# Optimization experiments

Measured on AMD Instinct MI355X. Metric: run time of the kernel, lower is better.

Reference implementation:

```python
import jax, jax.numpy as jnp
import numpy as np

N = 50000
E = 800000
IO = 128
HID = 256
KQ = 256
EPS = 1e-5


def setup_inputs() -> dict:
    key = jax.random.key(0)
    ks = jax.random.split(key, 16)
    def w(k, shape, fan_in):
        return jax.random.normal(k, shape, dtype=jnp.float32) / np.sqrt(fan_in)
    x0 = jax.random.normal(ks[0], (N, IO), dtype=jnp.float32)
    edges = jax.random.randint(ks[1], (2, E), 0, N, dtype=jnp.int64)
    return {
        "x0": x0,
        "edges": edges,
        "Wq1": w(ks[2], (IO, KQ), IO), "Wk1": w(ks[3], (IO, KQ), IO),
        "Wv1": w(ks[4], (IO, HID), IO), "Wr1": w(ks[5], (IO, HID), IO),
        "b1": jnp.zeros((HID,), jnp.float32),
        "g1": jnp.ones((HID,), jnp.float32), "be1": jnp.zeros((HID,), jnp.float32),
        "Wq2": w(ks[6], (HID, KQ), HID), "Wk2": w(ks[7], (HID, KQ), HID),
        "Wv2": w(ks[8], (HID, IO), HID), "Wr2": w(ks[9], (HID, IO), HID),
        "b2": jnp.zeros((IO,), jnp.float32),
        "g2": jnp.ones((IO,), jnp.float32), "be2": jnp.zeros((IO,), jnp.float32),
    }


def _transformer_conv(x, src, dst, Wq, Wk, Wv, Wr, b, n):
    # single-head graph transformer conv (PyG TransformerConv style)
    q = x @ Wq                      # [n, kq]
    k = x @ Wk                      # [n, kq]
    v = x @ Wv                      # [n, out]
    scale = 1.0 / np.sqrt(Wq.shape[1])
    logits = jnp.sum(q[dst] * k[src], axis=-1) * scale   # [E]
    m = jax.lax.stop_gradient(jax.ops.segment_max(logits, dst, num_segments=n))
    m = jnp.where(jnp.isfinite(m), m, 0.0)
    e = jnp.exp(logits - m[dst])                          # [E]
    s = jax.ops.segment_sum(e, dst, num_segments=n)       # [n]
    alpha = e / jnp.maximum(s[dst], 1e-16)                # [E]
    agg = jax.ops.segment_sum(alpha[:, None] * v[src], dst, num_segments=n)
    return agg + x @ Wr + b


def _batch_norm(x, gamma, beta):
    mu = jnp.mean(x, axis=0)
    var = jnp.mean((x - mu) ** 2, axis=0)  # biased var, as torch BN training
    return (x - mu) * jax.lax.rsqrt(var + EPS) * gamma + beta


def reference(x0, edges, Wq1, Wk1, Wv1, Wr1, b1, g1, be1,
              Wq2, Wk2, Wv2, Wr2, b2, g2, be2):
    src, dst = edges[0], edges[1]
    n = x0.shape[0]
    x = _transformer_conv(x0, src, dst, Wq1, Wk1, Wv1, Wr1, b1, n)
    x = jax.nn.relu(_batch_norm(x, g1, be1))
    x = _transformer_conv(x, src, dst, Wq2, Wk2, Wv2, Wr2, b2, n)
    x = _batch_norm(x, g2, be2)
    return jax.nn.relu(x + x0)
```

## Files before the change

### kernel.cpp

```cpp
#include <hip/hip_runtime.h>
#include <stdint.h>

typedef unsigned short ushort_t;

__device__ __forceinline__ float bf2f(unsigned short u) {
  union { unsigned int i; float f; } c; c.i = ((unsigned int)u) << 16; return c.f;
}
__device__ __forceinline__ unsigned short f2bf(float f) {
  union { float f; unsigned int i; } c; c.f = f;
  unsigned int r = c.i + 0x7FFFu + ((c.i >> 16) & 1u);
  return (unsigned short)(r >> 16);
}
__device__ __forceinline__ float relu_nanprop(float v) { return (v < 0.f) ? 0.f : v; }

__device__ __forceinline__ void async_copy16(const void* g, void* l) {
  __builtin_amdgcn_global_load_lds(
      (const __attribute__((address_space(1))) unsigned int*)(uintptr_t)g,
      (__attribute__((address_space(3))) unsigned int*)(uintptr_t)l,
      16, 0, 0);
}

typedef __attribute__((ext_vector_type(8))) short s16x8;
typedef __attribute__((ext_vector_type(4))) float f32x4;

__device__ __forceinline__ int edge_at(const void* edges, int wide, int idx) {
  if (wide) return (int)((const long long*)edges)[idx];
  return ((const int*)edges)[idx];
}

__global__ void setup_kernel(int* __restrict__ zreg2, int N,
                             const int* __restrict__ e32, int n32, int* __restrict__ eflag,
                             const unsigned int* __restrict__ x, int nw, int* __restrict__ fF) {
  int b = blockIdx.x, tid = threadIdx.x;
  if (b < 256) {
    int total = 2 * N + 1024;
    for (int i = b * 256 + tid; i < total; i += 256 * 256) zreg2[i] = 0;
  } else if (b == 256) {
    __shared__ int any;
    if (tid == 0) any = 0;
    __syncthreads();
    for (int i = tid; i < 4096; i += 256) {
      int idx = 2 * i + 1;
      if (idx < n32 && e32[idx] != 0) any = 1;
    }
    __syncthreads();
    if (tid == 0) eflag[0] = (any == 0) ? 1 : 0;
  } else {
    __shared__ int cnt;
    if (tid == 0) cnt = 0;
    __syncthreads();
    int local = 0;
    for (int i = tid; i < 4096 && i < nw; i += 256) {
      unsigned int low = x[i] & 0xFFFFu;
      unsigned int e = (low >> 7) & 0xFFu;
      if (low != 0u && (e < 96u || e > 144u)) local++;
    }
    atomicAdd(&cnt, local);
    __syncthreads();
    if (tid == 0) fF[0] = (cnt > 1024) ? 1 : 0;
  }
}

__global__ void cvt_all_kernel(const void* __restrict__ x0, ushort_t* __restrict__ x0b, int nx,
                               const void* p0, const void* p1, const void* p2,
                               const void* p3, const void* p4, const void* p5,
                               ushort_t* o0, ushort_t* o1, ushort_t* o2,
                               ushort_t* o3, ushort_t* o4, ushort_t* o5,
                               const void* W10, const void* W11, const void* W12, const void* W13,
                               ushort_t* __restrict__ Wq1b, ushort_t* __restrict__ Wk1b,
                               ushort_t* __restrict__ wcatB1, ushort_t* __restrict__ wcatV1,
                               const void* W20, const void* W21, const void* W22, const void* W23,
                               ushort_t* __restrict__ Wq2b, ushort_t* __restrict__ Wk2b,
                               ushort_t* __restrict__ wcatB2, ushort_t* __restrict__ wcatV2,
                               const void* __restrict__ edges, int* __restrict__ deg,
                               int E, int Nn,
                               const int* __restrict__ eflag, const int* __restrict__ fF) {
  int b = blockIdx.x, tid = threadIdx.x;
  int f = fF[0];
  if (b < 4096) {
    for (int i = b * 256 + tid; i < nx; i += 4096 * 256)
      x0b[i] = f ? f2bf(((const float*)x0)[i]) : ((const ushort_t*)x0)[i];
  } else if (b == 4096) {
    const void* ins[6] = {p0, p1, p2, p3, p4, p5};
    ushort_t* outs[6] = {o0, o1, o2, o3, o4, o5};
    const int segs[7] = {0, 256, 512, 768, 896, 1024, 1152};
    for (int i = tid; i < 1152; i += 256) {
      int s = 0;
      while (i >= segs[s + 1]) s++;
      int li = i - segs[s];
      outs[s][li] = f ? f2bf(((const float*)ins[s])[li]) : ((const ushort_t*)ins[s])[li];
    }
  } else if (b < 4609) {
    for (int i = (b - 4097) * 256 + tid; i < 131072; i += 512 * 256) {
      if (i < 32768) {
        Wq1b[i] = f ? f2bf(((const float*)W10)[i]) : ((const ushort_t*)W10)[i];
      } else if (i < 65536) {
        int r = i - 32768;
        Wk1b[r] = f ? f2bf(((const float*)W11)[r]) : ((const ushort_t*)W11)[r];
      } else if (i < 98304) {
        int rem = i - 65536, k = rem >> 8, c = rem & 255;
        ushort_t v = f ? f2bf(((const float*)W13)[rem]) : ((const ushort_t*)W13)[rem];
        wcatB1[(size_t)(128 + c) * 128 + k] = v;
      } else {
        int rem = i - 98304, k = rem >> 8, c = rem & 255;
        ushort_t v = f ? f2bf(((const float*)W12)[rem]) : ((const ushort_t*)W12)[rem];
        wcatV1[(size_t)c * 128 + k] = v;
      }
    }
  } else if (b < 5121) {
    for (int i = (b - 4609) * 256 + tid; i < 196608; i += 512 * 256) {
      if (i < 65536) {
        Wq2b[i] = f ? f2bf(((const float*)W20)[i]) : ((const ushort_t*)W20)[i];
      } else if (i < 131072) {
        int r = i - 65536;
        Wk2b[r] = f ? f2bf(((const float*)W21)[r]) : ((const ushort_t*)W21)[r];
      } else if (i < 163840) {
        int rem = i - 131072, k = rem >> 7, c = rem & 127;
        ushort_t v = f ? f2bf(((const float*)W23)[rem]) : ((const ushort_t*)W23)[rem];
        wcatB2[(size_t)(256 + c) * 256 + k] = v;
      } else {
        int rem = i - 163840, k = rem >> 7, c = rem & 127;
        ushort_t v = f ? f2bf(((const float*)W22)[rem]) : ((const ushort_t*)W22)[rem];
        wcatV2[(size_t)c * 256 + k] = v;
      }
    }
  } else {
    int wide = eflag[0];
    for (int e = (b - 5121) * 256 + tid; e < E; e += 1024 * 256) {
      int d = edge_at(edges, wide, E + e);
      if (d < 0) d = 0; if (d >= Nn) d = Nn - 1;
      atomicAdd(&deg[d], 1);
    }
  }
}

__global__ void chunk_sum_kernel(const int* __restrict__ deg, int* __restrict__ csum, int n) {
  int b = blockIdx.x, t = threadIdx.x, i = b * 256 + t;
  int v = (i < n) ? deg[i] : 0;
  __shared__ int ws[4];
#pragma unroll
  for (int o = 32; o > 0; o >>= 1) v += __shfl_down(v, o);
  if ((t & 63) == 0) ws[t >> 6] = v;
  __syncthreads();
  if (t == 0) csum[b] = ws[0] + ws[1] + ws[2] + ws[3];
}

__global__ void scan_small_kernel(const int* __restrict__ csum, int* __restrict__ cpre,
                                  int nc, int* __restrict__ offs, int N) {
  __shared__ int tmp[256];
  int t = threadIdx.x;
  int v = (t < nc) ? csum[t] : 0;
  tmp[t] = v;
  __syncthreads();
  for (int off = 1; off < 256; off <<= 1) {
    int x = (t >= off) ? tmp[t - off] : 0;
    __syncthreads();
    tmp[t] += x;
    __syncthreads();
  }
  if (t < nc) cpre[t] = tmp[t] - v;
  if (t == 255) offs[N] = tmp[255];
}

__global__ void scan_final_kernel(const int* __restrict__ deg, const int* __restrict__ cpre,
                                  int* __restrict__ offs, int n) {
  int b = blockIdx.x, t = threadIdx.x, i = b * 256 + t;
  __shared__ int tmp[256];
  int v = (i < n) ? deg[i] : 0;
  tmp[t] = v;
  __syncthreads();
  for (int off = 1; off < 256; off <<= 1) {
    int x = (t >= off) ? tmp[t - off] : 0;
    __syncthreads();
    tmp[t] += x;
    __syncthreads();
  }
  if (i < n) offs[i] = cpre[b] + tmp[t] - v;
}

__global__ void scatter_kernel(const void* __restrict__ edges, const int* __restrict__ flag,
                               const int* __restrict__ offs, int* __restrict__ fill,
                               int* __restrict__ srcS, int E, int Nn) {
  int wide = flag[0];
  for (int e = blockIdx.x * blockDim.x + threadIdx.x; e < E; e += gridDim.x * blockDim.x) {
    int s = edge_at(edges, wide, e);
    int d = edge_at(edges, wide, E + e);
    if (d < 0) d = 0; if (d >= Nn) d = Nn - 1;
    if (s < 0) s = 0; if (s >= Nn) s = Nn - 1;
    int p = offs[d] + atomicAdd(&fill[d], 1);
    if (p < 0) p = 0; if (p >= E) p = E - 1;
    srcS[p] = s;
  }
}

__global__ __launch_bounds__(256)
void gemm4_kernel(const ushort_t* __restrict__ A, const ushort_t* __restrict__ BT,
                  ushort_t* __restrict__ o0, ushort_t* __restrict__ o1,
                  ushort_t* __restrict__ o2, ushort_t* __restrict__ o3,
                  const ushort_t* __restrict__ bias3,
                  int M, int K, int NC, int b0, int b1, int b2, int accum) {
  __shared__ __align__(16) ushort_t As[128 * 32];
  __shared__ __align__(16) ushort_t Bs[128 * 32];
  int tid = threadIdx.x;
  int lane = tid & 63, wave = tid >> 6;
  int tm = blockIdx.x * 128, tn = blockIdx.y * 128;
  int wm = (wave >> 1) * 64, wn = (wave & 1) * 64;
  int q = lane >> 4, l = lane & 15;
  f32x4 acc[4][4];
#pragma unroll
  for (int a = 0; a < 4; a++)
#pragma unroll
    for (int b = 0; b < 4; b++) acc[a][b] = (f32x4){0.f, 0.f, 0.f, 0.f};

  int lrow = lane >> 2, c8 = (lane & 3) * 8;
  for (int k0 = 0; k0 < K; k0 += 32) {
#pragma unroll
    for (int t = 0; t < 2; t++) {
      int chunk = t * 4 + wave;
      int row = chunk * 16 + lrow;
      int ra = tm + row; if (ra > M - 1) ra = M - 1;
      async_copy16(&A[(size_t)ra * K + k0 + c8], &As[chunk * 512]);
      async_copy16(&BT[(size_t)(tn + row) * K + k0 + c8], &Bs[chunk * 512]);
    }
    __syncthreads();
    s16x8 af[4], bfr[4];
#pragma unroll
    for (int mf = 0; mf < 4; mf++) af[mf] = *(const s16x8*)&As[(wm + mf * 16 + l) * 32 + q * 8];
#pragma unroll
    for (int nf = 0; nf < 4; nf++) bfr[nf] = *(const s16x8*)&Bs[(wn + nf * 16 + l) * 32 + q * 8];
#pragma unroll
    for (int mf = 0; mf < 4; mf++)
#pragma unroll
      for (int nf = 0; nf < 4; nf++)
        acc[mf][nf] = __builtin_amdgcn_mfma_f32_16x16x32_bf16(af[mf], bfr[nf], acc[mf][nf], 0, 0, 0);
    __syncthreads();
  }
  ushort_t* op; int sbase, w; bool addb = false;
  if (tn < b0)      { op = o0; sbase = 0;  w = b0; }
  else if (tn < b1) { op = o1; sbase = b0; w = b1 - b0; }
  else if (tn < b2) { op = o2; sbase = b1; w = b2 - b1; }
  else              { op = o3; sbase = b2; w = NC - b2; addb = true; }
  int lc0 = tn + wn - sbase + l;
  float bv[4];
#pragma unroll
  for (int nf = 0; nf < 4; nf++) bv[nf] = addb ? bf2f(bias3[lc0 + nf * 16]) : 0.f;
#pragma unroll
  for (int mf = 0; mf < 4; mf++) {
#pragma unroll
    for (int j = 0; j < 4; j++) {
      int r = tm + wm + mf * 16 + q * 4 + j;
      if (r < M) {
#pragma unroll
        for (int nf = 0; nf < 4; nf++) {
          size_t idx = (size_t)r * w + lc0 + nf * 16;
          float prev = accum ? bf2f(op[idx]) : 0.f;
          op[idx] = f2bf(acc[mf][nf][j] + bv[nf] + prev);
        }
      }
    }
  }
}

__global__ __launch_bounds__(256)
void attn_kernel(const ushort_t* __restrict__ qt, const ushort_t* __restrict__ x,
                 const int* __restrict__ offs, const int* __restrict__ srcS,
                 ushort_t* __restrict__ aggb, int D, int Nn) {
  int lane = threadIdx.x & 63, wave = threadIdx.x >> 6;
  int n = blockIdx.x * 4 + wave;
  if (n >= Nn) return;
  int g = lane >> 4, sub = lane & 15;

  int e0 = offs[n], e1 = offs[n + 1];
  float wsum = 0.f;

  if (D == 128) {
    s16x8 qv = __builtin_nontemporal_load((const s16x8*)(qt + (size_t)n * 128 + sub * 8));
    float qf[8];
#pragma unroll
    for (int i = 0; i < 8; i++) qf[i] = bf2f((unsigned short)qv[i]);
    float acc[8];
#pragma unroll
    for (int i = 0; i < 8; i++) acc[i] = 0.f;
    int j = e0;
    s16x8 xc;
    bool have = (j + 4 <= e1);
    if (have) {
      int s = __builtin_nontemporal_load(srcS + j + g);
      if (s < 0 || s >= Nn) s = 0;
      xc = *(const s16x8*)(x + (size_t)s * 128 + sub * 8);
    }
    for (; j + 8 <= e1; j += 4) {
      int s2 = __builtin_nontemporal_load(srcS + j + 4 + g);
      if (s2 < 0 || s2 >= Nn) s2 = 0;
      s16x8 xn = *(const s16x8*)(x + (size_t)s2 * 128 + sub * 8);
      float p = 0.f;
#pragma unroll
      for (int i = 0; i < 8; i++) p += qf[i] * bf2f((unsigned short)xc[i]);
      p += __shfl_xor(p, 1); p += __shfl_xor(p, 2);
      p += __shfl_xor(p, 4); p += __shfl_xor(p, 8);
      float w = __expf(p * 0.0625f);
      wsum += w;
#pragma unroll
      for (int i = 0; i < 8; i++) acc[i] += w * bf2f((unsigned short)xc[i]);
      xc = xn;
    }
    if (have) {
      float p = 0.f;
#pragma unroll
      for (int i = 0; i < 8; i++) p += qf[i] * bf2f((unsigned short)xc[i]);
      p += __shfl_xor(p, 1); p += __shfl_xor(p, 2);
      p += __shfl_xor(p, 4); p += __shfl_xor(p, 8);
      float w = __expf(p * 0.0625f);
      wsum += w;
#pragma unroll
      for (int i = 0; i < 8; i++) acc[i] += w * bf2f((unsigned short)xc[i]);
      j += 4;
    }
    int rem = e1 - j;
    if (rem > 0) {
      bool valid = g < rem;
      int s = __builtin_nontemporal_load(srcS + (valid ? (j + g) : j));
      if (s < 0 || s >= Nn) s = 0;
      s16x8 xv = *(const s16x8*)(x + (size_t)s * 128 + sub * 8);
      float p = 0.f;
#pragma unroll
      for (int i = 0; i < 8; i++) p += qf[i] * bf2f((unsigned short)xv[i]);
      p += __shfl_xor(p, 1); p += __shfl_xor(p, 2);
      p += __shfl_xor(p, 4); p += __shfl_xor(p, 8);
      float w = 0.f;
      if (valid) w = __expf(p * 0.0625f);
      wsum += w;
#pragma unroll
      for (int i = 0; i < 8; i++) acc[i] += w * bf2f((unsigned short)xv[i]);
    }
    wsum += __shfl_xor(wsum, 16); wsum += __shfl_xor(wsum, 32);
#pragma unroll
    for (int i = 0; i < 8; i++) {
      acc[i] += __shfl_xor(acc[i], 16);
      acc[i] += __shfl_xor(acc[i], 32);
    }
    float inv = 1.f / fmaxf(wsum, 1e-16f);
    if (g == 0) {
      s16x8 r0;
#pragma unroll
      for (int i = 0; i < 8; i++) r0[i] = (short)f2bf(acc[i] * inv);
      *(s16x8*)(aggb + (size_t)n * 128 + sub * 8) = r0;
    }
  } else {
    s16x8 q0 = __builtin_nontemporal_load((const s16x8*)(qt + (size_t)n * 256 + sub * 16));
    s16x8 q1 = __builtin_nontemporal_load((const s16x8*)(qt + (size_t)n * 256 + sub * 16 + 8));
    float qf[16];
#pragma unroll
    for (int i = 0; i < 8; i++) {
      qf[i]     = bf2f((unsigned short)q0[i]);
      qf[8 + i] = bf2f((unsigned short)q1[i]);
    }
    float acc[16];
#pragma unroll
    for (int i = 0; i < 16; i++) acc[i] = 0.f;
    int j = e0;
    s16x8 x0c, x1c;
    bool have = (j + 4 <= e1);
    if (have) {
      int s = __builtin_nontemporal_load(srcS + j + g);
      if (s < 0 || s >= Nn) s = 0;
      const ushort_t* xp = x + (size_t)s * 256 + sub * 16;
      x0c = *(const s16x8*)xp; x1c = *(const s16x8*)(xp + 8);
    }
    for (; j + 8 <= e1; j += 4) {
      int s2 = __builtin_nontemporal_load(srcS + j + 4 + g);
      if (s2 < 0 || s2 >= Nn) s2 = 0;
      const ushort_t* xp2 = x + (size_t)s2 * 256 + sub * 16;
      s16x8 x0n = *(const s16x8*)xp2, x1n = *(const s16x8*)(xp2 + 8);
      float pa = 0.f, pb = 0.f;
#pragma unroll
      for (int i = 0; i < 8; i++) {
        pa += qf[i] * bf2f((unsigned short)x0c[i]);
        pb += qf[8 + i] * bf2f((unsigned short)x1c[i]);
      }
      float p = pa + pb;
      p += __shfl_xor(p, 1); p += __shfl_xor(p, 2);
      p += __shfl_xor(p, 4); p += __shfl_xor(p, 8);
      float w = __expf(p * 0.0625f);
      wsum += w;
#pragma unroll
      for (int i = 0; i < 8; i++) {
        acc[i]     += w * bf2f((unsigned short)x0c[i]);
        acc[8 + i] += w * bf2f((unsigned short)x1c[i]);
      }
      x0c = x0n; x1c = x1n;
    }
    if (have) {
      float pa = 0.f, pb = 0.f;
#pragma unroll
      for (int i = 0; i < 8; i++) {
        pa += qf[i] * bf2f((unsigned short)x0c[i]);
        pb += qf[8 + i] * bf2f((unsigned short)x1c[i]);
      }
      float p = pa + pb;
      p += __shfl_xor(p, 1); p += __shfl_xor(p, 2);
      p += __shfl_xor(p, 4); p += __shfl_xor(p, 8);
      float w = __expf(p * 0.0625f);
      wsum += w;
#pragma unroll
      for (int i = 0; i < 8; i++) {
        acc[i]     += w * bf2f((unsigned short)x0c[i]);
        acc[8 + i] += w * bf2f((unsigned short)x1c[i]);
      }
      j += 4;
    }
    int rem = e1 - j;
    if (rem > 0) {
      bool valid = g < rem;
      int s = __builtin_nontemporal_load(srcS + (valid ? (j + g) : j));
      if (s < 0 || s >= Nn) s = 0;
      const ushort_t* xp = x + (size_t)s * 256 + sub * 16;
      s16x8 x0v = *(const s16x8*)xp, x1v = *(const s16x8*)(xp + 8);
      float pa = 0.f, pb = 0.f;
#pragma unroll
      for (int i = 0; i < 8; i++) {
        pa += qf[i] * bf2f((unsigned short)x0v[i]);
        pb += qf[8 + i] * bf2f((unsigned short)x1v[i]);
      }
      float p = pa + pb;
      p += __shfl_xor(p, 1); p += __shfl_xor(p, 2);
      p += __shfl_xor(p, 4); p += __shfl_xor(p, 8);
      float w = 0.f;
      if (valid) w = __expf(p * 0.0625f);
      wsum += w;
#pragma unroll
      for (int i = 0; i < 8; i++) {
        acc[i]     += w * bf2f((unsigned short)x0v[i]);
        acc[8 + i] += w * bf2f((unsigned short)x1v[i]);
      }
    }
    wsum += __shfl_xor(wsum, 16); wsum += __shfl_xor(wsum, 32);
#pragma unroll
    for (int i = 0; i < 16; i++) {
      acc[i] += __shfl_xor(acc[i], 16);
      acc[i] += __shfl_xor(acc[i], 32);
    }
    float inv = 1.f / fmaxf(wsum, 1e-16f);
    if (g == 0) {
      s16x8 r0, r1;
#pragma unroll
      for (int i = 0; i < 8; i++) {
        r0[i] = (short)f2bf(acc[i] * inv);
        r1[i] = (short)f2bf(acc[8 + i] * inv);
      }
      size_t idx = (size_t)n * 256 + sub * 16;
      *(s16x8*)(aggb + idx) = r0;
      *(s16x8*)(aggb + idx + 8) = r1;
    }
  }
}

__global__ void bn_stats_kernel(const ushort_t* __restrict__ h, float* __restrict__ sum,
                                float* __restrict__ sumsq, int N, int F) {
  int col = threadIdx.x;
  float s = 0.f, s2 = 0.f;
  for (int r = blockIdx.x; r < N; r += gridDim.x) {
    float x = bf2f(h[(size_t)r * F + col]);
    s += x; s2 += x * x;
  }
  atomicAdd(&sum[col], s);
  atomicAdd(&sumsq[col], s2);
}

__global__ void norm_relu_kernel(const ushort_t* __restrict__ h,
                                 const float* __restrict__ sum, const float* __restrict__ sumsq,
                                 const ushort_t* __restrict__ g, const ushort_t* __restrict__ be,
                                 ushort_t* __restrict__ x1, int N, size_t total, int cmask) {
  __shared__ float sc[256], sh[256];
  int t = threadIdx.x;
  if (t <= cmask) {
    float mu = sum[t] / (float)N;
    float var = sumsq[t] / (float)N - mu * mu;
    float s = bf2f(g[t]) * rsqrtf(var + 1e-5f);
    sc[t] = s;
    sh[t] = bf2f(be[t]) - mu * s;
  }
  __syncthreads();
  for (size_t i = blockIdx.x * (size_t)blockDim.x + t; i < total;
       i += (size_t)gridDim.x * blockDim.x) {
    int c = (int)(i & (size_t)cmask);
    float vv = bf2f(h[i]) * sc[c] + sh[c];
    x1[i] = f2bf(relu_nanprop(vv));
  }
}

__global__ void final_kernel(const ushort_t* __restrict__ h,
                             const float* __restrict__ sum, const float* __restrict__ sumsq,
                             const ushort_t* __restrict__ g, const ushort_t* __restrict__ be,
                             const ushort_t* __restrict__ x0b, void* __restrict__ out,
                             const int* __restrict__ flagF, int N, size_t total) {
  __shared__ float sc[128], sh[128];
  int t = threadIdx.x;
  if (t < 128) {
    float mu = sum[t] / (float)N;
    float var = sumsq[t] / (float)N - mu * mu;
    float s = bf2f(g[t]) * rsqrtf(var + 1e-5f);
    sc[t] = s;
    sh[t] = bf2f(be[t]) - mu * s;
  }
  __syncthreads();
  int f = flagF[0];
  for (size_t i = blockIdx.x * (size_t)blockDim.x + t; i < total;
       i += (size_t)gridDim.x * blockDim.x) {
    int c = (int)(i & 127);
    float vv = bf2f(h[i]) * sc[c] + sh[c] + bf2f(x0b[i]);
    vv = relu_nanprop(vv);
    if (f) ((float*)out)[i] = vv;
    else   ((ushort_t*)out)[i] = f2bf(vv);
  }
}

extern "C" void kernel_launch(void* const* d_in, const int* in_sizes, int n_in,
                              void* d_out, int out_size, void* d_ws, size_t ws_size,
                              hipStream_t stream) {
  const void* x0  = d_in[0];
  const void* edges = d_in[1];
  const void* Wq1 = d_in[2];
  const void* Wk1 = d_in[3];
  const void* Wv1 = d_in[4];
  const void* Wr1 = d_in[5];
  const void* b1  = d_in[6];
  const void* gw1 = d_in[7];
  const void* bw1 = d_in[8];
  const void* Wq2 = d_in[9];
  const void* Wk2 = d_in[10];
  const void* Wv2 = d_in[11];
  const void* Wr2 = d_in[12];
  const void* b2  = d_in[13];
  const void* gw2 = d_in[14];
  const void* bw2 = d_in[15];

  int N = in_sizes[0] / 128;
  int E = in_sizes[1] / 2;
  int NCHUNK = (N + 255) / 256;
  int MT = (N + 127) / 128;

  uintptr_t base = (uintptr_t)d_ws;
  auto carve = [&](size_t bytes) -> void* {
    uintptr_t p = base;
    base += (bytes + 255) & ~(size_t)255;
    return (void*)p;
  };
  ushort_t* x0b = (ushort_t*)carve((size_t)N * 128 * 2);
  ushort_t* qtb = (ushort_t*)carve((size_t)N * 256 * 2);
  ushort_t* aggb = (ushort_t*)carve((size_t)N * 256 * 2);
  ushort_t* hb = (ushort_t*)carve((size_t)N * 256 * 2);
  ushort_t* x1 = (ushort_t*)carve((size_t)N * 256 * 2);
  ushort_t* Wq1b = (ushort_t*)carve((size_t)128 * 256 * 2);
  ushort_t* Wk1b = (ushort_t*)carve((size_t)128 * 256 * 2);
  ushort_t* wcatB1 = (ushort_t*)carve((size_t)384 * 128 * 2);
  ushort_t* wcatV1 = (ushort_t*)carve((size_t)256 * 128 * 2);
  ushort_t* Wq2b = (ushort_t*)carve((size_t)256 * 256 * 2);
  ushort_t* Wk2b = (ushort_t*)carve((size_t)256 * 256 * 2);
  ushort_t* wcatB2 = (ushort_t*)carve((size_t)384 * 256 * 2);
  ushort_t* wcatV2 = (ushort_t*)carve((size_t)128 * 256 * 2);
  ushort_t* b1b  = (ushort_t*)carve(256 * 2);
  ushort_t* g1b  = (ushort_t*)carve(256 * 2);
  ushort_t* be1b = (ushort_t*)carve(256 * 2);
  ushort_t* b2b  = (ushort_t*)carve(128 * 2);
  ushort_t* g2b  = (ushort_t*)carve(128 * 2);
  ushort_t* be2b = (ushort_t*)carve(128 * 2);
  int* offs = (int*)carve((size_t)(N + 1) * 4);
  int* srcS = (int*)carve((size_t)E * 4);
  int* csum = (int*)carve(256 * 4);
  int* cpre = (int*)carve(256 * 4);
  int nzero = 2 * N + 1024;
  int* zreg2 = (int*)carve((size_t)nzero * 4);
  int* deg   = zreg2;
  int* fill  = zreg2 + N;
  float* sum1 = (float*)(zreg2 + 2 * N);
  float* sq1  = sum1 + 256;
  float* sum2 = sum1 + 512;
  float* sq2  = sum1 + 640;
  int* eflag = (int*)carve(256);
  int* fF = eflag + 1;

  size_t needed = base - (uintptr_t)d_ws;
  if (needed > ws_size) return;

  setup_kernel<<<258, 256, 0, stream>>>(zreg2, N, (const int*)edges, 2 * E, eflag,
                                        (const unsigned int*)x0, N * 128, fF);
  cvt_all_kernel<<<6145, 256, 0, stream>>>(x0, x0b, N * 128,
                                           b1, gw1, bw1, b2, gw2, bw2,
                                           b1b, g1b, be1b, b2b, g2b, be2b,
                                           Wq1, Wk1, Wv1, Wr1, Wq1b, Wk1b, wcatB1, wcatV1,
                                           Wq2, Wk2, Wv2, Wr2, Wq2b, Wk2b, wcatB2, wcatV2,
                                           edges, deg, E, N, eflag, fF);
  chunk_sum_kernel<<<NCHUNK, 256, 0, stream>>>(deg, csum, N);
  scan_small_kernel<<<1, 256, 0, stream>>>(csum, cpre, NCHUNK, offs, N);
  scan_final_kernel<<<NCHUNK, 256, 0, stream>>>(deg, cpre, offs, N);
  scatter_kernel<<<1024, 256, 0, stream>>>(edges, eflag, offs, fill, srcS, E, N);

  gemm4_kernel<<<dim3(1, 1), 256, 0, stream>>>(Wk1b, Wq1b, wcatB1, wcatB1, wcatB1, wcatB1,
                                               b1b, 128, 256, 128, 128, 128, 128, 0);
  gemm4_kernel<<<dim3(2, 2), 256, 0, stream>>>(Wk2b, Wq2b, wcatB2, wcatB2, wcatB2, wcatB2,
                                               b1b, 256, 256, 256, 256, 256, 256, 0);

  int gAttn = (N + 3) / 4;
  gemm4_kernel<<<dim3(MT, 3), 256, 0, stream>>>(x0b, wcatB1, qtb, qtb, qtb, hb, b1b,
                                                N, 128, 384, 128, 128, 128, 0);
  attn_kernel<<<gAttn, 256, 0, stream>>>(qtb, x0b, offs, srcS, aggb, 128, N);
  gemm4_kernel<<<dim3(MT, 2), 256, 0, stream>>>(aggb, wcatV1, hb, hb, hb, hb, b1b,
                                                N, 128, 256, 256, 256, 256, 1);
  bn_stats_kernel<<<512, 256, 0, stream>>>(hb, sum1, sq1, N, 256);
  norm_relu_kernel<<<4096, 256, 0, stream>>>(hb, sum1, sq1, g1b, be1b, x1, N,
                                             (size_t)N * 256, 255);
  gemm4_kernel<<<dim3(MT, 3), 256, 0, stream>>>(x1, wcatB2, qtb, qtb, qtb, hb, b2b,
                                                N, 256, 384, 256, 256, 256, 0);
  attn_kernel<<<gAttn, 256, 0, stream>>>(qtb, x1, offs, srcS, aggb, 256, N);
  gemm4_kernel<<<dim3(MT, 1), 256, 0, stream>>>(aggb, wcatV2, hb, hb, hb, hb, b1b,
                                                N, 256, 128, 128, 128, 128, 1);
  bn_stats_kernel<<<512, 128, 0, stream>>>(hb, sum2, sq2, N, 128);
  final_kernel<<<4096, 256, 0, stream>>>(hb, sum2, sq2, g2b, be2b, x0b, d_out, fF, N,
                                         (size_t)N * 128);
}
```

Before: 548.3 us.

## Fuse root and value projections into one K-concatenated GEMM

The root projection x@Wr and the aggregated-value projection agg@Wv become a single GEMM over the concatenated inputs [x | agg] against a stacked weight [Wr ; Wv]. The GEMM kernel gains a second A pointer and a K split point, and the read-modify-write accumulate path is dropped. The query GEMM shrinks to produce only the q-transformed columns. This removes one write and one read of the hidden buffer per layer, at the cost of a branch on the A source inside the K loop.

```diff
diff --git a/kernel.cpp b/kernel.cpp
--- a/kernel.cpp
+++ b/kernel.cpp
@@ -68,10 +68,10 @@
                                ushort_t* o3, ushort_t* o4, ushort_t* o5,
                                const void* W10, const void* W11, const void* W12, const void* W13,
                                ushort_t* __restrict__ Wq1b, ushort_t* __restrict__ Wk1b,
-                               ushort_t* __restrict__ wcatB1, ushort_t* __restrict__ wcatV1,
+                               ushort_t* __restrict__ wcatH1,
                                const void* W20, const void* W21, const void* W22, const void* W23,
                                ushort_t* __restrict__ Wq2b, ushort_t* __restrict__ Wk2b,
-                               ushort_t* __restrict__ wcatB2, ushort_t* __restrict__ wcatV2,
+                               ushort_t* __restrict__ wcatH2,
                                const void* __restrict__ edges, int* __restrict__ deg,
                                int E, int Nn,
                                const int* __restrict__ eflag, const int* __restrict__ fF) {
@@ -100,11 +100,11 @@
       } else if (i < 98304) {
         int rem = i - 65536, k = rem >> 8, c = rem & 255;
         ushort_t v = f ? f2bf(((const float*)W13)[rem]) : ((const ushort_t*)W13)[rem];
-        wcatB1[(size_t)(128 + c) * 128 + k] = v;
+        wcatH1[(size_t)c * 256 + k] = v;
       } else {
         int rem = i - 98304, k = rem >> 8, c = rem & 255;
         ushort_t v = f ? f2bf(((const float*)W12)[rem]) : ((const ushort_t*)W12)[rem];
-        wcatV1[(size_t)c * 128 + k] = v;
+        wcatH1[(size_t)c * 256 + 128 + k] = v;
       }
     }
   } else if (b < 5121) {
@@ -117,11 +117,11 @@
       } else if (i < 163840) {
         int rem = i - 131072, k = rem >> 7, c = rem & 127;
         ushort_t v = f ? f2bf(((const float*)W23)[rem]) : ((const ushort_t*)W23)[rem];
-        wcatB2[(size_t)(256 + c) * 256 + k] = v;
+        wcatH2[(size_t)c * 512 + k] = v;
       } else {
         int rem = i - 163840, k = rem >> 7, c = rem & 127;
         ushort_t v = f ? f2bf(((const float*)W22)[rem]) : ((const ushort_t*)W22)[rem];
-        wcatV2[(size_t)c * 256 + k] = v;
+        wcatH2[(size_t)c * 512 + 256 + k] = v;
       }
     }
   } else {
@@ -194,11 +194,13 @@
 }
 
 __global__ __launch_bounds__(256)
-void gemm4_kernel(const ushort_t* __restrict__ A, const ushort_t* __restrict__ BT,
+void gemm4_kernel(const ushort_t* __restrict__ A, const ushort_t* __restrict__ A2,
+                  int Ksplit,
+                  const ushort_t* __restrict__ BT,
                   ushort_t* __restrict__ o0, ushort_t* __restrict__ o1,
                   ushort_t* __restrict__ o2, ushort_t* __restrict__ o3,
                   const ushort_t* __restrict__ bias3,
-                  int M, int K, int NC, int b0, int b1, int b2, int accum) {
+                  int M, int K, int NC, int b0, int b1, int b2) {
   __shared__ __align__(16) ushort_t As[128 * 32];
   __shared__ __align__(16) ushort_t Bs[128 * 32];
   int tid = threadIdx.x;
@@ -214,12 +216,15 @@
 
   int lrow = lane >> 2, c8 = (lane & 3) * 8;
   for (int k0 = 0; k0 < K; k0 += 32) {
+    const ushort_t* Ap; int kk, sA;
+    if (k0 < Ksplit) { Ap = A;  kk = k0;          sA = Ksplit; }
+    else             { Ap = A2; kk = k0 - Ksplit; sA = K - Ksplit; }
 #pragma unroll
     for (int t = 0; t < 2; t++) {
       int chunk = t * 4 + wave;
       int row = chunk * 16 + lrow;
       int ra = tm + row; if (ra > M - 1) ra = M - 1;
-      async_copy16(&A[(size_t)ra * K + k0 + c8], &As[chunk * 512]);
+      async_copy16(&Ap[(size_t)ra * sA + kk + c8], &As[chunk * 512]);
       async_copy16(&BT[(size_t)(tn + row) * K + k0 + c8], &Bs[chunk * 512]);
     }
     __syncthreads();
@@ -251,11 +256,8 @@
       int r = tm + wm + mf * 16 + q * 4 + j;
       if (r < M) {
 #pragma unroll
-        for (int nf = 0; nf < 4; nf++) {
-          size_t idx = (size_t)r * w + lc0 + nf * 16;
-          float prev = accum ? bf2f(op[idx]) : 0.f;
-          op[idx] = f2bf(acc[mf][nf][j] + bv[nf] + prev);
-        }
+        for (int nf = 0; nf < 4; nf++)
+          op[(size_t)r * w + lc0 + nf * 16] = f2bf(acc[mf][nf][j] + bv[nf]);
       }
     }
   }
@@ -553,12 +555,12 @@
   ushort_t* x1 = (ushort_t*)carve((size_t)N * 256 * 2);
   ushort_t* Wq1b = (ushort_t*)carve((size_t)128 * 256 * 2);
   ushort_t* Wk1b = (ushort_t*)carve((size_t)128 * 256 * 2);
-  ushort_t* wcatB1 = (ushort_t*)carve((size_t)384 * 128 * 2);
-  ushort_t* wcatV1 = (ushort_t*)carve((size_t)256 * 128 * 2);
+  ushort_t* wcatQ1 = (ushort_t*)carve((size_t)128 * 128 * 2);
+  ushort_t* wcatH1 = (ushort_t*)carve((size_t)256 * 256 * 2);
   ushort_t* Wq2b = (ushort_t*)carve((size_t)256 * 256 * 2);
   ushort_t* Wk2b = (ushort_t*)carve((size_t)256 * 256 * 2);
-  ushort_t* wcatB2 = (ushort_t*)carve((size_t)384 * 256 * 2);
-  ushort_t* wcatV2 = (ushort_t*)carve((size_t)128 * 256 * 2);
+  ushort_t* wcatQ2 = (ushort_t*)carve((size_t)256 * 256 * 2);
+  ushort_t* wcatH2 = (ushort_t*)carve((size_t)128 * 512 * 2);
   ushort_t* b1b  = (ushort_t*)carve(256 * 2);
   ushort_t* g1b  = (ushort_t*)carve(256 * 2);
   ushort_t* be1b = (ushort_t*)carve(256 * 2);
@@ -588,33 +590,39 @@
   cvt_all_kernel<<<6145, 256, 0, stream>>>(x0, x0b, N * 128,
                                            b1, gw1, bw1, b2, gw2, bw2,
                                            b1b, g1b, be1b, b2b, g2b, be2b,
-                                           Wq1, Wk1, Wv1, Wr1, Wq1b, Wk1b, wcatB1, wcatV1,
-                                           Wq2, Wk2, Wv2, Wr2, Wq2b, Wk2b, wcatB2, wcatV2,
+                                           Wq1, Wk1, Wv1, Wr1, Wq1b, Wk1b, wcatH1,
+                                           Wq2, Wk2, Wv2, Wr2, Wq2b, Wk2b, wcatH2,
                                            edges, deg, E, N, eflag, fF);
   chunk_sum_kernel<<<NCHUNK, 256, 0, stream>>>(deg, csum, N);
   scan_small_kernel<<<1, 256, 0, stream>>>(csum, cpre, NCHUNK, offs, N);
   scan_final_kernel<<<NCHUNK, 256, 0, stream>>>(deg, cpre, offs, N);
   scatter_kernel<<<1024, 256, 0, stream>>>(edges, eflag, offs, fill, srcS, E, N);
 
-  gemm4_kernel<<<dim3(1, 1), 256, 0, stream>>>(Wk1b, Wq1b, wcatB1, wcatB1, wcatB1, wcatB1,
-                                               b1b, 128, 256, 128, 128, 128, 128, 0);
-  gemm4_kernel<<<dim3(2, 2), 256, 0, stream>>>(Wk2b, Wq2b, wcatB2, wcatB2, wcatB2, wcatB2,
-                                               b1b, 256, 256, 256, 256, 256, 256, 0);
+  gemm4_kernel<<<dim3(1, 1), 256, 0, stream>>>(Wk1b, Wk1b, 256, Wq1b,
+                                               wcatQ1, wcatQ1, wcatQ1, wcatQ1,
+                                               b1b, 128, 256, 128, 128, 128, 128);
+  gemm4_kernel<<<dim3(2, 2), 256, 0, stream>>>(Wk2b, Wk2b, 256, Wq2b,
+                                               wcatQ2, wcatQ2, wcatQ2, wcatQ2,
+                                               b1b, 256, 256, 256, 256, 256, 256);
 
   int gAttn = (N + 3) / 4;
-  gemm4_kernel<<<dim3(MT, 3), 256, 0, stream>>>(x0b, wcatB1, qtb, qtb, qtb, hb, b1b,
-                                                N, 128, 384, 128, 128, 128, 0);
+  gemm4_kernel<<<dim3(MT, 1), 256, 0, stream>>>(x0b, x0b, 128, wcatQ1,
+                                                qtb, qtb, qtb, qtb,
+                                                b1b, N, 128, 128, 128, 128, 128);
   attn_kernel<<<gAttn, 256, 0, stream>>>(qtb, x0b, offs, srcS, aggb, 128, N);
-  gemm4_kernel<<<dim3(MT, 2), 256, 0, stream>>>(aggb, wcatV1, hb, hb, hb, hb, b1b,
-                                                N, 128, 256, 256, 256, 256, 1);
+  gemm4_kernel<<<dim3(MT, 2), 256, 0, stream>>>(x0b, aggb, 128, wcatH1,
+                                                hb, hb, hb, hb,
+                                                b1b, N, 256, 256, 0, 0, 0);
   bn_stats_kernel<<<512, 256, 0, stream>>>(hb, sum1, sq1, N, 256);
   norm_relu_kernel<<<4096, 256, 0, stream>>>(hb, sum1, sq1, g1b, be1b, x1, N,
                                              (size_t)N * 256, 255);
-  gemm4_kernel<<<dim3(MT, 3), 256, 0, stream>>>(x1, wcatB2, qtb, qtb, qtb, hb, b2b,
-                                                N, 256, 384, 256, 256, 256, 0);
+  gemm4_kernel<<<dim3(MT, 2), 256, 0, stream>>>(x1, x1, 256, wcatQ2,
+                                                qtb, qtb, qtb, qtb,
+                                                b2b, N, 256, 256, 256, 256, 256);
   attn_kernel<<<gAttn, 256, 0, stream>>>(qtb, x1, offs, srcS, aggb, 256, N);
-  gemm4_kernel<<<dim3(MT, 1), 256, 0, stream>>>(aggb, wcatV2, hb, hb, hb, hb, b1b,
-                                                N, 256, 128, 128, 128, 128, 1);
+  gemm4_kernel<<<dim3(MT, 1), 256, 0, stream>>>(x1, aggb, 256, wcatH2,
+                                                hb, hb, hb, hb,
+                                                b2b, N, 512, 128, 0, 0, 0);
   bn_stats_kernel<<<512, 128, 0, stream>>>(hb, sum2, sq2, N, 128);
   final_kernel<<<4096, 256, 0, stream>>>(hb, sum2, sq2, g2b, be2b, x0b, d_out, fF, N,
                                          (size_t)N * 128);
```

Measured after the change: 507.3 us. 7.5% less time.
